# Kernel optimization log

Hardware: AMD Instinct MI355X
Metric: run time of the kernel (lower is better)

Reference implementation:

```python
import jax, jax.numpy as jnp
import numpy as np

B, S, IN, N, MOT = 128, 4096, 6, 64, 3
ODE_UNFOLDS = 6
EPS = 1e-8


def setup_inputs() -> dict:
    ks = jax.random.split(jax.random.key(0), 20)
    u = lambda k, shape, lo, hi: jax.random.uniform(k, shape, jnp.float32, lo, hi)
    pm1 = lambda k, shape: jnp.where(jax.random.bernoulli(k, 0.5, shape), 1.0, -1.0).astype(jnp.float32)
    return {
        "x": jax.random.normal(ks[0], (B, S, IN), jnp.float32),
        "mean_us": 0.1 * jax.random.normal(ks[1], (IN,), jnp.float32),
        "std_us": u(ks[2], (IN,), 0.5, 1.5),
        "input_w": u(ks[3], (IN,), 0.8, 1.2),
        "input_b": 0.01 * jax.random.normal(ks[4], (IN,), jnp.float32),
        "output_w": u(ks[5], (MOT,), 0.8, 1.2),
        "output_b": 0.01 * jax.random.normal(ks[6], (MOT,), jnp.float32),
        "gleak": u(ks[7], (N,), 0.001, 1.0),
        "vleak": u(ks[8], (N,), -0.2, 0.2),
        "cm": u(ks[9], (N,), 0.4, 0.6),
        "sensory_W": u(ks[10], (IN, N), 0.001, 1.0),
        "sensory_mu": u(ks[11], (IN, N), 0.3, 0.8),
        "sensory_sigma": u(ks[12], (IN, N), 3.0, 8.0),
        "sensory_erev": pm1(ks[13], (IN, N)),
        "W": u(ks[14], (N, N), 0.001, 1.0),
        "mu": u(ks[15], (N, N), 0.3, 0.8),
        "sigma": u(ks[16], (N, N), 3.0, 8.0),
        "erev": pm1(ks[17], (N, N)),
    }


def _ltc_sequence(x, mean_us, std_us, input_w, input_b, output_w, output_b,
                  gleak, vleak, cm, sensory_W, sensory_mu, sensory_sigma,
                  sensory_erev, W, mu, sigma, erev):
    # normalize inputs (DgaRawSequence) then LTCCell input mapping
    xn = (x - mean_us) / std_us                      # [B,S,IN]
    xm = xn * input_w + input_b                      # [B,S,IN]
    cm_t = cm * ODE_UNFOLDS                          # cm / (elapsed_time=1 / ode_unfolds)

    def step(v, u_t):                                # v: [B,N], u_t: [B,IN]
        # sensory synapse activations [B,IN,N]
        s_act = sensory_W * jax.nn.sigmoid((u_t[:, :, None] - sensory_mu) * sensory_sigma)
        wns = jnp.sum(s_act * sensory_erev, axis=1)  # [B,N]
        wds = jnp.sum(s_act, axis=1)                 # [B,N]
        for _ in range(ODE_UNFOLDS):
            w_act = W * jax.nn.sigmoid((v[:, :, None] - mu) * sigma)  # [B,N,N]
            num = cm_t * v + gleak * vleak + jnp.sum(w_act * erev, axis=1) + wns
            den = cm_t + gleak + jnp.sum(w_act, axis=1) + wds
            v = num / (den + EPS)
        return v, v

    v0 = jnp.zeros((x.shape[0], gleak.shape[0]), dtype=x.dtype)
    _, vs = jax.lax.scan(step, v0, jnp.swapaxes(xm, 0, 1))   # [S,B,N]
    states = jnp.swapaxes(vs, 0, 1)                          # [B,S,N]
    # LTCCell output mapping (motor neurons = first MOT states)
    out = states[..., :MOT] * output_w + output_b            # [B,S,3]
    # denormalize (DgaRawSequence)
    return out * std_us[:MOT] + mean_us[:MOT]


def reference(x, mean_us, std_us, input_w, input_b, output_w, output_b,
              gleak, vleak, cm, sensory_W, sensory_mu, sensory_sigma,
              sensory_erev, W, mu, sigma, erev):
    return _ltc_sequence(x, mean_us, std_us, input_w, input_b, output_w,
                         output_b, gleak, vleak, cm, sensory_W, sensory_mu,
                         sensory_sigma, sensory_erev, W, mu, sigma, erev)
```

## Files before the change

kernel.cpp:

```cpp
#include <hip/hip_runtime.h>

#define B_ 128
#define S_ 4096
#define IN_ 6
#define N_ 64
#define MOT_ 3
#define UNF 6
#define EPS_ 1e-8f
#define LOG2E 1.4426950408889634f

__device__ __forceinline__ float bperm(int addr, float v) {
    return __int_as_float(__builtin_amdgcn_ds_bpermute(addr, __float_as_int(v)));
}

__launch_bounds__(512, 1)
__global__ void ltc_kernel(
    const float* __restrict__ x,
    const float* __restrict__ mean_us, const float* __restrict__ std_us,
    const float* __restrict__ input_w, const float* __restrict__ input_b,
    const float* __restrict__ output_w, const float* __restrict__ output_b,
    const float* __restrict__ gleak, const float* __restrict__ vleak,
    const float* __restrict__ cm,
    const float* __restrict__ sW, const float* __restrict__ sMu,
    const float* __restrict__ sSig, const float* __restrict__ sErev,
    const float* __restrict__ W, const float* __restrict__ Mu,
    const float* __restrict__ Sig, const float* __restrict__ Erev,
    float* __restrict__ out)
{
    const int b    = blockIdx.x;
    const int t    = threadIdx.x;
    const int lane = t & 63;
    const int w    = t >> 6;
    const int cc   = lane >> 3;
    const int ii   = lane & 7;
    const int myCol = w * 8 + ii;
    const int jb   = cc * 8;

    __shared__ __align__(16) float vbuf[2][N_];
    __shared__ float s_lds[IN_][N_][2];

    float A[8], Bc[8], Wr[8], We[8];
#pragma unroll
    for (int jj = 0; jj < 8; ++jj) {
        int idx = (jb + jj) * N_ + myCol;
        float sg = Sig[idx], m = Mu[idx], ww = W[idx], e = Erev[idx];
        A[jj]  = -sg * LOG2E;
        Bc[jj] = m * sg * LOG2E;
        Wr[jj] = ww;
        We[jj] = ww * e;
    }

    const float cmt = cm[myCol] * (float)UNF;
    const float glk = gleak[myCol];
    const float gv  = glk * vleak[myCol];

    float SA = 0.f, SB = 0.f, SWv = 0.f, SWe = 0.f, nscale = 0.f, nbias = 0.f;
    if (w < IN_) {
        int idx = w * N_ + lane;
        float sg = sSig[idx], m = sMu[idx], ww = sW[idx], e = sErev[idx];
        SA  = -sg * LOG2E;
        SB  = m * sg * LOG2E;
        SWv = ww;
        SWe = ww * e;
        nscale = input_w[w] / std_us[w];
        nbias  = input_b[w] - mean_us[w] / std_us[w] * input_w[w];
    }

    float OW = 0.f, OB = 0.f;
    if (t < MOT_) {
        OW = output_w[t] * std_us[t];
        OB = output_b[t] * std_us[t] + mean_us[t];
    }

    const float* xb = x + (size_t)b * S_ * IN_;
    float* ob = out + (size_t)b * S_ * MOT_;

    if (t < N_) vbuf[0][t] = 0.f;
    if (w < IN_) {
        float u  = xb[w] * nscale + nbias;
        float e  = __builtin_amdgcn_exp2f(u * SA + SB);
        float sg = __builtin_amdgcn_rcpf(1.0f + e);
        s_lds[w][lane][0] = SWe * sg;
        s_lds[w][lane][1] = SWv * sg;
    }
    __syncthreads();

    const int bp8  = (lane ^ 8)  << 2;
    const int bp16 = (lane ^ 16) << 2;
    const int bp32 = (lane ^ 32) << 2;

    float v_my = 0.f, nb = 0.f, db = 0.f, xnext = 0.f;

    for (int s = 0; s < S_; ++s) {
        if (w < IN_) xnext = xb[((s + 1 < S_) ? (s + 1) : s) * IN_ + w];

#pragma unroll
        for (int k = 0; k < UNF; ++k) {
            const int p = k & 1;
            float4 va = *(const float4*)&vbuf[p][jb];
            float4 vc = *(const float4*)&vbuf[p][jb + 4];
            const float vj[8] = {va.x, va.y, va.z, va.w, vc.x, vc.y, vc.z, vc.w};

            float pn = 0.f, pd = 0.f;
#pragma unroll
            for (int jj = 0; jj < 8; ++jj) {
                float e  = __builtin_amdgcn_exp2f(vj[jj] * A[jj] + Bc[jj]);
                float sg = __builtin_amdgcn_rcpf(1.0f + e);
                pn += We[jj] * sg;
                pd += Wr[jj] * sg;
            }
            pn += bperm(bp8,  pn);  pd += bperm(bp8,  pd);
            pn += bperm(bp16, pn);  pd += bperm(bp16, pd);
            pn += bperm(bp32, pn);  pd += bperm(bp32, pd);

            if (k == 0) {
                float a = 0.f, d = 0.f;
#pragma unroll
                for (int ci = 0; ci < IN_; ++ci) {
                    a += s_lds[ci][myCol][0];
                    d += s_lds[ci][myCol][1];
                }
                nb = gv + a;
                db = cmt + glk + d + EPS_;
            }

            float num = cmt * v_my + nb + pn;
            v_my = num * __builtin_amdgcn_rcpf(db + pd);

            if (cc == 0) vbuf[p ^ 1][w * 8 + ii] = v_my;

            if (k == UNF - 1 && w < IN_) {
                float u  = xnext * nscale + nbias;
                float e2 = __builtin_amdgcn_exp2f(u * SA + SB);
                float sg = __builtin_amdgcn_rcpf(1.0f + e2);
                s_lds[w][lane][0] = SWe * sg;
                s_lds[w][lane][1] = SWv * sg;
            }
            __syncthreads();
        }

        if (t < MOT_) ob[s * MOT_ + t] = v_my * OW + OB;
    }
}

extern "C" void kernel_launch(void* const* d_in, const int* in_sizes, int n_in,
                              void* d_out, int out_size, void* d_ws, size_t ws_size,
                              hipStream_t stream) {
    (void)in_sizes; (void)n_in; (void)d_ws; (void)ws_size; (void)out_size;
    const float* x       = (const float*)d_in[0];
    const float* mean_us = (const float*)d_in[1];
    const float* std_us  = (const float*)d_in[2];
    const float* input_w = (const float*)d_in[3];
    const float* input_b = (const float*)d_in[4];
    const float* out_w   = (const float*)d_in[5];
    const float* out_b   = (const float*)d_in[6];
    const float* gleak   = (const float*)d_in[7];
    const float* vleak   = (const float*)d_in[8];
    const float* cm      = (const float*)d_in[9];
    const float* sW      = (const float*)d_in[10];
    const float* sMu     = (const float*)d_in[11];
    const float* sSig    = (const float*)d_in[12];
    const float* sErev   = (const float*)d_in[13];
    const float* W       = (const float*)d_in[14];
    const float* Mu      = (const float*)d_in[15];
    const float* Sig     = (const float*)d_in[16];
    const float* Erev    = (const float*)d_in[17];
    float* out = (float*)d_out;

    ltc_kernel<<<dim3(B_), dim3(512), 0, stream>>>(
        x, mean_us, std_us, input_w, input_b, out_w, out_b,
        gleak, vleak, cm, sW, sMu, sSig, sErev, W, Mu, Sig, Erev, out);
}
```

Baseline: 11.22 ms.

## Use DPP/permlane reductions, LDS-only barriers, and earlier sensory update

```diff
diff --git a/kernel.cpp b/kernel.cpp
--- a/kernel.cpp
+++ b/kernel.cpp
@@ -9,8 +9,33 @@
 #define EPS_ 1e-8f
 #define LOG2E 1.4426950408889634f
 
-__device__ __forceinline__ float bperm(int addr, float v) {
-    return __int_as_float(__builtin_amdgcn_ds_bpermute(addr, __float_as_int(v)));
+__device__ __forceinline__ float red8(float x) {
+    int r = __builtin_amdgcn_update_dpp(0, __float_as_int(x), 0x128 ,
+                                        0xF, 0xF, true);
+    return x + __int_as_float(r);
+}
+__device__ __forceinline__ float red16(float x) {
+#if __has_builtin(__builtin_amdgcn_permlane16_swap)
+    auto r = __builtin_amdgcn_permlane16_swap(__float_as_int(x), __float_as_int(x),
+                                              false, false);
+    return __int_as_float((int)r[0]) + __int_as_float((int)r[1]);
+#else
+    return x + __shfl_xor(x, 16, 64);
+#endif
+}
+__device__ __forceinline__ float red32(float x) {
+#if __has_builtin(__builtin_amdgcn_permlane32_swap)
+    auto r = __builtin_amdgcn_permlane32_swap(__float_as_int(x), __float_as_int(x),
+                                              false, false);
+    return __int_as_float((int)r[0]) + __int_as_float((int)r[1]);
+#else
+    return x + __shfl_xor(x, 32, 64);
+#endif
+}
+
+__device__ __forceinline__ void lds_barrier() {
+    asm volatile("s_waitcnt lgkmcnt(0)" ::: "memory");
+    __builtin_amdgcn_s_barrier();
 }
 
 __launch_bounds__(512, 1)
@@ -53,6 +78,7 @@
     const float cmt = cm[myCol] * (float)UNF;
     const float glk = gleak[myCol];
     const float gv  = glk * vleak[myCol];
+    const float dbase = cmt + glk + EPS_;
 
     float SA = 0.f, SB = 0.f, SWv = 0.f, SWe = 0.f, nscale = 0.f, nbias = 0.f;
     if (w < IN_) {
@@ -77,22 +103,28 @@
 
     if (t < N_) vbuf[0][t] = 0.f;
     if (w < IN_) {
-        float u  = xb[w] * nscale + nbias;
-        float e  = __builtin_amdgcn_exp2f(u * SA + SB);
+        float u  = fmaf(xb[w], nscale, nbias);
+        float e  = __builtin_amdgcn_exp2f(fmaf(u, SA, SB));
         float sg = __builtin_amdgcn_rcpf(1.0f + e);
         s_lds[w][lane][0] = SWe * sg;
         s_lds[w][lane][1] = SWv * sg;
     }
-    __syncthreads();
+    lds_barrier();
 
-    const int bp8  = (lane ^ 8)  << 2;
-    const int bp16 = (lane ^ 16) << 2;
-    const int bp32 = (lane ^ 32) << 2;
-
-    float v_my = 0.f, nb = 0.f, db = 0.f, xnext = 0.f;
+    float v_my = 0.f;
 
     for (int s = 0; s < S_; ++s) {
+        float xnext = 0.f;
         if (w < IN_) xnext = xb[((s + 1 < S_) ? (s + 1) : s) * IN_ + w];
+
+        float a = 0.f, d = 0.f;
+#pragma unroll
+        for (int ci = 0; ci < IN_; ++ci) {
+            float2 sv = *(const float2*)&s_lds[ci][myCol][0];
+            a += sv.x; d += sv.y;
+        }
+        const float nb = gv + a;
+        const float db = dbase + d;
 
 #pragma unroll
         for (int k = 0; k < UNF; ++k) {
@@ -104,42 +136,31 @@
             float pn = 0.f, pd = 0.f;
 #pragma unroll
             for (int jj = 0; jj < 8; ++jj) {
-                float e  = __builtin_amdgcn_exp2f(vj[jj] * A[jj] + Bc[jj]);
+                float e  = __builtin_amdgcn_exp2f(fmaf(vj[jj], A[jj], Bc[jj]));
                 float sg = __builtin_amdgcn_rcpf(1.0f + e);
-                pn += We[jj] * sg;
-                pd += Wr[jj] * sg;
+                pn = fmaf(We[jj], sg, pn);
+                pd = fmaf(Wr[jj], sg, pd);
             }
-            pn += bperm(bp8,  pn);  pd += bperm(bp8,  pd);
-            pn += bperm(bp16, pn);  pd += bperm(bp16, pd);
-            pn += bperm(bp32, pn);  pd += bperm(bp32, pd);
+            pn = red8(pn);   pd = red8(pd);
+            pn = red16(pn);  pd = red16(pd);
+            pn = red32(pn);  pd = red32(pd);
 
-            if (k == 0) {
-                float a = 0.f, d = 0.f;
-#pragma unroll
-                for (int ci = 0; ci < IN_; ++ci) {
-                    a += s_lds[ci][myCol][0];
-                    d += s_lds[ci][myCol][1];
-                }
-                nb = gv + a;
-                db = cmt + glk + d + EPS_;
-            }
-
-            float num = cmt * v_my + nb + pn;
+            float num = fmaf(cmt, v_my, nb + pn);
             v_my = num * __builtin_amdgcn_rcpf(db + pd);
 
-            if (cc == 0) vbuf[p ^ 1][w * 8 + ii] = v_my;
+            if (cc == 0) vbuf[p ^ 1][myCol] = v_my;
 
-            if (k == UNF - 1 && w < IN_) {
-                float u  = xnext * nscale + nbias;
-                float e2 = __builtin_amdgcn_exp2f(u * SA + SB);
+            if (k == 1 && w < IN_) {
+                float u  = fmaf(xnext, nscale, nbias);
+                float e2 = __builtin_amdgcn_exp2f(fmaf(u, SA, SB));
                 float sg = __builtin_amdgcn_rcpf(1.0f + e2);
                 s_lds[w][lane][0] = SWe * sg;
                 s_lds[w][lane][1] = SWv * sg;
             }
-            __syncthreads();
+            lds_barrier();
         }
 
-        if (t < MOT_) ob[s * MOT_ + t] = v_my * OW + OB;
+        if (t < MOT_) ob[s * MOT_ + t] = fmaf(v_my, OW, OB);
     }
 }
 
```

New measurement: 10.41 ms. -7.3%, faster.
